# Kernel optimization log

Hardware: AMD Instinct MI355X
Metric: run time of the kernel (lower is better)

The kernel has to match this reference:

```python
import jax, jax.numpy as jnp
import numpy as np

N_NODES = 50000
N_EDGES = 800000
N_GRAPHS = 256
D = 256
L = 3
BN_EPS = 1e-5


def setup_inputs() -> dict:
    key = jax.random.key(0)
    ks = jax.random.split(key, 8)
    x = jax.random.normal(ks[0], (N_NODES, D), dtype=jnp.float32)
    edge_index = jax.random.randint(ks[1], (2, N_EDGES), 0, N_NODES, dtype=jnp.int64)
    batch = jnp.sort(jax.random.randint(ks[2], (N_NODES,), 0, N_GRAPHS, dtype=jnp.int64))
    # small init scale keeps ReLU/BN chain numerically tame
    w1 = jax.random.normal(ks[3], (L, D, D), dtype=jnp.float32) * 0.05
    b1 = jnp.zeros((L, D), dtype=jnp.float32)
    w2 = jax.random.normal(ks[4], (L, D, D), dtype=jnp.float32) * 0.05
    b2 = jnp.zeros((L, D), dtype=jnp.float32)
    gamma = jnp.ones((L, D), dtype=jnp.float32)
    beta = jnp.zeros((L, D), dtype=jnp.float32)
    return {"x": x, "edge_index": edge_index, "batch": batch,
            "w1": w1, "b1": b1, "w2": w2, "b2": b2,
            "gamma": gamma, "beta": beta}


def reference(x, edge_index, batch, w1, b1, w2, b2, gamma, beta):
    src = edge_index[0]  # message senders (x_j)
    dst = edge_index[1]  # aggregation targets (x_i)
    h = x
    xs = []
    for i in range(L):
        # GINConv (eps=0): MLP(x_i + sum_{j in N(i)} x_j)
        agg = jax.ops.segment_sum(h[src], dst, num_segments=N_NODES)  # [N, D]
        z = h + agg
        z = jnp.maximum(z @ w1[i] + b1[i], 0.0) @ w2[i] + b2[i]  # Linear-ReLU-Linear
        z = jnp.maximum(z, 0.0)  # F.relu after conv
        # BatchNorm1d (training mode: biased batch stats over nodes)
        mean = jnp.mean(z, axis=0)
        var = jnp.var(z, axis=0)
        z = (z - mean) * jax.lax.rsqrt(var + BN_EPS) * gamma[i] + beta[i]
        xs.append(z)
        h = z
    # global_add_pool per layer, then concat along features -> [G, L*D]
    pooled = [jax.ops.segment_sum(xi, batch, num_segments=N_GRAPHS) for xi in xs]
    return jnp.concatenate(pooled, axis=1)
```

## Files before the change

kernel.cpp:

```cpp
#include <hip/hip_runtime.h>

#define NN 50000
#define NE 800000
#define NG 256
#define DD 256
#define NL 3
#define BN_EPS 1e-5f
#define MPAD 50048
#define CAP 96
#define NMB 391

typedef short bf16x8 __attribute__((ext_vector_type(8)));
typedef float f32x4 __attribute__((ext_vector_type(4)));
typedef unsigned short ushort8 __attribute__((ext_vector_type(8)));

__device__ __forceinline__ unsigned short f2bf(float f) {
    unsigned int u = __float_as_uint(f);
    u += 0x7FFFu + ((u >> 16) & 1u);
    return (unsigned short)(u >> 16);
}
__device__ __forceinline__ float bf2f(unsigned short s) {
    return __uint_as_float(((unsigned int)s) << 16);
}

__global__ void k_init(int* __restrict__ deg) {
    int i = blockIdx.x * blockDim.x + threadIdx.x;
    if (i < NN) deg[i] = 0;
}

__global__ void k_scatter(const int* __restrict__ ei, int* __restrict__ deg,
                          unsigned short* __restrict__ elist) {
    int e = blockIdx.x * blockDim.x + threadIdx.x;
    if (e >= NE) return;
    int s = ei[e];
    int d = ei[NE + e];
    int pos = atomicAdd(&deg[d], 1);
    elist[(size_t)d * CAP + pos] = (unsigned short)s;
}

__global__ void k_gbounds(const int* __restrict__ batch, int* __restrict__ gstart) {
    int g = threadIdx.x;
    int lo = 0, hi = NN;
    while (lo < hi) {
        int mid = (lo + hi) >> 1;
        if (batch[mid] < g) lo = mid + 1; else hi = mid;
    }
    gstart[g] = lo;
    if (g == 0) gstart[NG] = NN;
}

__global__ void k_f2bf(const float* __restrict__ in, unsigned short* __restrict__ out, int n4) {
    int i = blockIdx.x * blockDim.x + threadIdx.x;
    if (i >= n4) return;
    float4 v = ((const float4*)in)[i];
    ushort4 o;
    o.x = f2bf(v.x); o.y = f2bf(v.y); o.z = f2bf(v.z); o.w = f2bf(v.w);
    ((ushort4*)out)[i] = o;
}

__global__ void k_zrow(unsigned short* __restrict__ hbf) {
    hbf[(size_t)NN * DD + threadIdx.x] = 0;
}

__global__ void k_zpad(unsigned short* p) {
    int i = blockIdx.x * blockDim.x + threadIdx.x;
    const int total = (MPAD - NN) * DD;
    if (i < total) p[NN * DD + i] = 0;
}

__global__ void k_wconv(const float* __restrict__ w1, const float* __restrict__ w2,
                        unsigned short* __restrict__ wt) {
    int flat = blockIdx.x * blockDim.x + threadIdx.x;
    if (flat >= 6 * 65536) return;
    int mat = flat >> 16;
    int n = (flat >> 8) & 255;
    int k = flat & 255;
    const float* src = (mat < 3) ? (w1 + ((size_t)mat << 16)) : (w2 + ((size_t)(mat - 3) << 16));
    wt[flat] = f2bf(src[k * 256 + n]);
}

__global__ __launch_bounds__(256) void k_agg_bf(const unsigned short* __restrict__ h,
                                                const int* __restrict__ deg,
                                                const unsigned short* __restrict__ elist,
                                                unsigned short* __restrict__ z0) {
    int wave = threadIdx.x >> 6;
    int lane = threadIdx.x & 63;
    int node = blockIdx.x * 4 + wave;
    int chunk = lane & 31;
    int half = lane >> 5;
    const ushort8* h8 = (const ushort8*)h;

    float acc[8];
    if (half == 0) {
        ushort8 own = h8[(size_t)node * 32 + chunk];
        #pragma unroll
        for (int j = 0; j < 8; ++j) acc[j] = bf2f(own[j]);
    } else {
        #pragma unroll
        for (int j = 0; j < 8; ++j) acc[j] = 0.f;
    }

    int n = deg[node];
    const unsigned short* el = elist + (size_t)node * CAP;
    int i = 0;
    for (; i + 8 <= n; i += 8) {
        ushort8 sv = *(const ushort8*)(el + i);
        int i0 = half ? sv[1] : sv[0];
        int i1 = half ? sv[3] : sv[2];
        int i2 = half ? sv[5] : sv[4];
        int i3 = half ? sv[7] : sv[6];
        ushort8 r0 = h8[(size_t)i0 * 32 + chunk];
        ushort8 r1 = h8[(size_t)i1 * 32 + chunk];
        ushort8 r2 = h8[(size_t)i2 * 32 + chunk];
        ushort8 r3 = h8[(size_t)i3 * 32 + chunk];
        #pragma unroll
        for (int j = 0; j < 8; ++j) acc[j] += bf2f(r0[j]);
        #pragma unroll
        for (int j = 0; j < 8; ++j) acc[j] += bf2f(r1[j]);
        #pragma unroll
        for (int j = 0; j < 8; ++j) acc[j] += bf2f(r2[j]);
        #pragma unroll
        for (int j = 0; j < 8; ++j) acc[j] += bf2f(r3[j]);
    }
    for (; i < n; i += 2) {
        int s0 = el[i];
        int s1 = (i + 1 < n) ? (int)el[i + 1] : NN;
        int idx = half ? s1 : s0;
        ushort8 r = h8[(size_t)idx * 32 + chunk];
        #pragma unroll
        for (int j = 0; j < 8; ++j) acc[j] += bf2f(r[j]);
    }

    ushort8 o;
    #pragma unroll
    for (int j = 0; j < 8; ++j) {
        float other = __shfl_xor(acc[j], 32);
        o[j] = f2bf(acc[j] + other);
    }
    if (half == 0) ((ushort8*)z0)[(size_t)node * 32 + chunk] = o;
}

__global__ __launch_bounds__(512, 2) void k_mlp(const unsigned short* __restrict__ A,
                                                const unsigned short* __restrict__ BT1,
                                                const unsigned short* __restrict__ BT2,
                                                const float* __restrict__ b1,
                                                const float* __restrict__ b2,
                                                float* __restrict__ Cout,
                                                float* __restrict__ pstat) {
    __shared__ short As[128 * 64];
    __shared__ short Bs[256 * 64];
    __shared__ short H1[128 * 256];
    __shared__ float spart[2][256][2];
    int tid = threadIdx.x;
    int lane = tid & 63;
    int wave = tid >> 6;
    int wr = wave >> 2, wc = wave & 3;
    long m0 = (long)blockIdx.x * 128;
    const int r = lane & 15, hi = lane >> 4;

    f32x4 acc[4][4];
    #pragma unroll
    for (int m = 0; m < 4; ++m)
        #pragma unroll
        for (int n = 0; n < 4; ++n)
            acc[m][n] = (f32x4){0.f, 0.f, 0.f, 0.f};

    for (int k0 = 0; k0 < DD; k0 += 64) {
        #pragma unroll
        for (int p = 0; p < 2; ++p) {
            int flat = p * 512 + tid;
            int row = flat >> 3, c8 = flat & 7;
            int slot = c8 ^ (row & 7);
            *(bf16x8*)(As + row * 64 + slot * 8) =
                *(const bf16x8*)(A + (m0 + row) * DD + k0 + c8 * 8);
        }
        #pragma unroll
        for (int p = 0; p < 4; ++p) {
            int flat = p * 512 + tid;
            int row = flat >> 3, c8 = flat & 7;
            int slot = c8 ^ (row & 7);
            *(bf16x8*)(Bs + row * 64 + slot * 8) =
                *(const bf16x8*)(BT1 + (long)row * DD + k0 + c8 * 8);
        }
        __syncthreads();
        bf16x8 af[4][2], bfr[4][2];
        #pragma unroll
        for (int m = 0; m < 4; ++m) {
            int row = wr * 64 + m * 16 + r;
            #pragma unroll
            for (int kk = 0; kk < 2; ++kk) {
                int slot = (kk * 4 + hi) ^ (row & 7);
                af[m][kk] = *(const bf16x8*)(As + row * 64 + slot * 8);
            }
        }
        #pragma unroll
        for (int n = 0; n < 4; ++n) {
            int col = wc * 64 + n * 16 + r;
            #pragma unroll
            for (int kk = 0; kk < 2; ++kk) {
                int slot = (kk * 4 + hi) ^ (col & 7);
                bfr[n][kk] = *(const bf16x8*)(Bs + col * 64 + slot * 8);
            }
        }
        #pragma unroll
        for (int kk = 0; kk < 2; ++kk)
            #pragma unroll
            for (int m = 0; m < 4; ++m)
                #pragma unroll
                for (int n = 0; n < 4; ++n)
                    acc[m][n] = __builtin_amdgcn_mfma_f32_16x16x32_bf16(af[m][kk], bfr[n][kk], acc[m][n], 0, 0, 0);
        __syncthreads();
    }

    #pragma unroll
    for (int n = 0; n < 4; ++n) {
        int col = wc * 64 + n * 16 + r;
        float bv = b1[col];
        int g = col >> 3, j8 = col & 7;
        #pragma unroll
        for (int m = 0; m < 4; ++m) {
            #pragma unroll
            for (int j = 0; j < 4; ++j) {
                int row = wr * 64 + m * 16 + hi * 4 + j;
                float v = acc[m][n][j] + bv;
                v = v > 0.f ? v : 0.f;
                H1[row * 256 + (g ^ (row & 7)) * 8 + j8] = (short)f2bf(v);
            }
        }
    }
    #pragma unroll
    for (int m = 0; m < 4; ++m)
        #pragma unroll
        for (int n = 0; n < 4; ++n)
            acc[m][n] = (f32x4){0.f, 0.f, 0.f, 0.f};
    __syncthreads();

    for (int k0 = 0; k0 < DD; k0 += 64) {
        #pragma unroll
        for (int p = 0; p < 4; ++p) {
            int flat = p * 512 + tid;
            int row = flat >> 3, c8 = flat & 7;
            int slot = c8 ^ (row & 7);
            *(bf16x8*)(Bs + row * 64 + slot * 8) =
                *(const bf16x8*)(BT2 + (long)row * DD + k0 + c8 * 8);
        }
        __syncthreads();
        bf16x8 af[4][2], bfr[4][2];
        #pragma unroll
        for (int m = 0; m < 4; ++m) {
            int row = wr * 64 + m * 16 + r;
            #pragma unroll
            for (int kk = 0; kk < 2; ++kk) {
                int g = (k0 >> 3) + kk * 4 + hi;
                af[m][kk] = *(const bf16x8*)(H1 + row * 256 + (g ^ (row & 7)) * 8);
            }
        }
        #pragma unroll
        for (int n = 0; n < 4; ++n) {
            int col = wc * 64 + n * 16 + r;
            #pragma unroll
            for (int kk = 0; kk < 2; ++kk) {
                int slot = (kk * 4 + hi) ^ (col & 7);
                bfr[n][kk] = *(const bf16x8*)(Bs + col * 64 + slot * 8);
            }
        }
        #pragma unroll
        for (int kk = 0; kk < 2; ++kk)
            #pragma unroll
            for (int m = 0; m < 4; ++m)
                #pragma unroll
                for (int n = 0; n < 4; ++n)
                    acc[m][n] = __builtin_amdgcn_mfma_f32_16x16x32_bf16(af[m][kk], bfr[n][kk], acc[m][n], 0, 0, 0);
        __syncthreads();
    }

    #pragma unroll
    for (int n = 0; n < 4; ++n) {
        int col = wc * 64 + n * 16 + r;
        float bv = b2[col];
        float cs = 0.f, cs2 = 0.f;
        #pragma unroll
        for (int m = 0; m < 4; ++m) {
            #pragma unroll
            for (int j = 0; j < 4; ++j) {
                long grow = m0 + wr * 64 + m * 16 + hi * 4 + j;
                float v = acc[m][n][j] + bv;
                v = v > 0.f ? v : 0.f;
                Cout[grow * DD + col] = v;
                float vm = (grow < NN) ? v : 0.f;
                cs += vm; cs2 += vm * vm;
            }
        }
        cs  += __shfl_xor(cs, 16);  cs  += __shfl_xor(cs, 32);
        cs2 += __shfl_xor(cs2, 16); cs2 += __shfl_xor(cs2, 32);
        if (hi == 0) {
            spart[wr][col][0] = cs;
            spart[wr][col][1] = cs2;
        }
    }
    __syncthreads();
    if (tid < 256) {
        float s  = spart[0][tid][0] + spart[1][tid][0];
        float s2 = spart[0][tid][1] + spart[1][tid][1];
        pstat[(size_t)blockIdx.x * 512 + tid] = s;
        pstat[(size_t)blockIdx.x * 512 + 256 + tid] = s2;
    }
}

__global__ __launch_bounds__(256) void k_bnscale2(const float* __restrict__ pstat,
                                                  const float* __restrict__ gamma,
                                                  const float* __restrict__ beta,
                                                  float* __restrict__ ss) {
    int c = blockIdx.x;
    int t = threadIdx.x;
    float s = 0.f, s2 = 0.f;
    for (int mb = t; mb < NMB; mb += 256) {
        s  += pstat[(size_t)mb * 512 + c];
        s2 += pstat[(size_t)mb * 512 + 256 + c];
    }
    __shared__ float rs[256], rs2[256];
    rs[t] = s; rs2[t] = s2;
    __syncthreads();
    #pragma unroll
    for (int d = 128; d > 0; d >>= 1) {
        if (t < d) { rs[t] += rs[t + d]; rs2[t] += rs2[t + d]; }
        __syncthreads();
    }
    if (t == 0) {
        float mean = rs[0] * (1.0f / NN);
        float var = rs2[0] * (1.0f / NN) - mean * mean;
        float sc = gamma[c] * rsqrtf(var + BN_EPS);
        ss[c] = sc;
        ss[DD + c] = beta[c] - mean * sc;
    }
}

__global__ __launch_bounds__(512) void k_bnpool(const float* __restrict__ z,
                                                const float* __restrict__ ss,
                                                const int* __restrict__ gstart,
                                                unsigned short* __restrict__ hbf,
                                                float* __restrict__ out, int layer) {
    __shared__ float4 red[8][64];
    int g = blockIdx.x;
    int t = threadIdx.x;
    int q = t & 63, rg = t >> 6;
    float4 sc = ((const float4*)ss)[q];
    float4 sh = ((const float4*)(ss + DD))[q];
    int lo = gstart[g], hi = gstart[g + 1];
    float4 s = {0.f, 0.f, 0.f, 0.f};
    const float4* z4 = (const float4*)z;
    ushort4* h4 = (ushort4*)hbf;
    for (int r = lo + rg; r < hi; r += 8) {
        float4 v = z4[r * 64 + q];
        v.x = v.x * sc.x + sh.x;
        v.y = v.y * sc.y + sh.y;
        v.z = v.z * sc.z + sh.z;
        v.w = v.w * sc.w + sh.w;
        s.x += v.x; s.y += v.y; s.z += v.z; s.w += v.w;
        ushort4 o;
        o.x = f2bf(v.x); o.y = f2bf(v.y); o.z = f2bf(v.z); o.w = f2bf(v.w);
        h4[r * 64 + q] = o;
    }
    red[rg][q] = s;
    __syncthreads();
    if (rg < 4) {
        float4 a = red[rg][q], b = red[rg + 4][q];
        a.x += b.x; a.y += b.y; a.z += b.z; a.w += b.w;
        red[rg][q] = a;
    }
    __syncthreads();
    if (rg < 2) {
        float4 a = red[rg][q], b = red[rg + 2][q];
        a.x += b.x; a.y += b.y; a.z += b.z; a.w += b.w;
        red[rg][q] = a;
    }
    __syncthreads();
    if (rg == 0) {
        float4 a = red[0][q], b = red[1][q];
        a.x += b.x; a.y += b.y; a.z += b.z; a.w += b.w;
        ((float4*)(out + (size_t)g * (NL * DD) + layer * DD))[q] = a;
    }
}

extern "C" void kernel_launch(void* const* d_in, const int* in_sizes, int n_in,
                              void* d_out, int out_size, void* d_ws, size_t ws_size,
                              hipStream_t stream) {
    const float* x     = (const float*)d_in[0];
    const int*   ei    = (const int*)d_in[1];
    const int*   batch = (const int*)d_in[2];
    const float* w1    = (const float*)d_in[3];
    const float* b1    = (const float*)d_in[4];
    const float* w2    = (const float*)d_in[5];
    const float* b2    = (const float*)d_in[6];
    const float* gamma = (const float*)d_in[7];
    const float* beta  = (const float*)d_in[8];
    float* out = (float*)d_out;

    char* ws = (char*)d_ws;
    size_t off = 0;
    auto alloc = [&](size_t bytes) -> void* {
        void* p = ws + off;
        off += (bytes + 255) & ~size_t(255);
        return p;
    };
    float*          buf0 = (float*)alloc((size_t)MPAD * DD * 4);
    unsigned short* zbf  = (unsigned short*)alloc((size_t)MPAD * DD * 2);
    unsigned short* hbf  = (unsigned short*)alloc((size_t)(NN + 64) * DD * 2);
    unsigned short* wt   = (unsigned short*)alloc((size_t)6 * DD * DD * 2);
    int* deg    = (int*)alloc((size_t)NN * 4);
    unsigned short* elist = (unsigned short*)alloc((size_t)NN * CAP * 2);
    int* gstart = (int*)alloc((size_t)(NG + 1) * 4);
    float* pstat = (float*)alloc((size_t)NMB * 512 * 4);
    float* ss   = (float*)alloc(2 * DD * 4);

    k_init<<<(NN + 255) / 256, 256, 0, stream>>>(deg);
    k_scatter<<<(NE + 255) / 256, 256, 0, stream>>>(ei, deg, elist);
    k_gbounds<<<1, 256, 0, stream>>>(batch, gstart);

    k_wconv<<<(6 * 65536 + 255) / 256, 256, 0, stream>>>(w1, w2, wt);
    k_f2bf<<<(NN * DD / 4 + 255) / 256, 256, 0, stream>>>(x, hbf, NN * DD / 4);
    k_zrow<<<1, 256, 0, stream>>>(hbf);
    k_zpad<<<((MPAD - NN) * DD + 255) / 256, 256, 0, stream>>>(zbf);

    for (int l = 0; l < NL; ++l) {
        k_agg_bf<<<NN / 4, 256, 0, stream>>>(hbf, deg, elist, zbf);
        k_mlp<<<NMB, 512, 0, stream>>>(zbf, wt + (size_t)l * DD * DD,
                                       wt + (size_t)(3 + l) * DD * DD,
                                       b1 + l * DD, b2 + l * DD, buf0, pstat);
        k_bnscale2<<<DD, 256, 0, stream>>>(pstat, gamma + l * DD, beta + l * DD, ss);
        k_bnpool<<<NG, 512, 0, stream>>>(buf0, ss, gstart, hbf, out, l);
    }
}
```

Baseline: 419.9 us.

## Fuse setup kernels, split aggregation by feature halves, widen bnpool grid

Merges the separate setup kernels (bf16 conversion, weight transpose, zeroing, graph bounds) into one launch to cut launch overhead. Aggregation now runs as two launches, each covering half of the feature columns with four edges gathered in parallel per wave, so each pass touches a smaller working set of h that may fit better in cache. The BN+pool kernel uses a 2D grid over graph and feature half, and the final layer skips writing the bf16 hidden state that no later kernel reads. The cost is a second pass over the edge lists, extra shuffle reductions, and one more launch per layer.

```diff
diff --git a/kernel.cpp b/kernel.cpp
--- a/kernel.cpp
+++ b/kernel.cpp
@@ -23,9 +23,53 @@
     return __uint_as_float(((unsigned int)s) << 16);
 }
 
-__global__ void k_init(int* __restrict__ deg) {
+#define R0 3200000
+#define R1 393216
+#define R2 50000
+#define R3 12288
+#define R4 256
+#define R5 256
+#define RTOT (R0 + R1 + R2 + R3 + R4 + R5)
+
+__global__ void k_setup(const float* __restrict__ x, const float* __restrict__ w1,
+                        const float* __restrict__ w2, const int* __restrict__ batch,
+                        unsigned short* __restrict__ hbf, unsigned short* __restrict__ wt,
+                        int* __restrict__ deg, unsigned short* __restrict__ zbf,
+                        int* __restrict__ gstart) {
     int i = blockIdx.x * blockDim.x + threadIdx.x;
-    if (i < NN) deg[i] = 0;
+    if (i < R0) {
+        float4 v = ((const float4*)x)[i];
+        ushort4 o;
+        o.x = f2bf(v.x); o.y = f2bf(v.y); o.z = f2bf(v.z); o.w = f2bf(v.w);
+        ((ushort4*)hbf)[i] = o;
+        return;
+    }
+    i -= R0;
+    if (i < R1) {
+        int mat = i >> 16;
+        int n = (i >> 8) & 255;
+        int k = i & 255;
+        const float* src = (mat < 3) ? (w1 + ((size_t)mat << 16)) : (w2 + ((size_t)(mat - 3) << 16));
+        wt[i] = f2bf(src[k * 256 + n]);
+        return;
+    }
+    i -= R1;
+    if (i < R2) { deg[i] = 0; return; }
+    i -= R2;
+    if (i < R3) { zbf[NN * DD + i] = 0; return; }
+    i -= R3;
+    if (i < R4) { hbf[(size_t)NN * DD + i] = 0; return; }
+    i -= R4;
+    if (i < R5) {
+        int g = i;
+        int lo = 0, hi = NN;
+        while (lo < hi) {
+            int mid = (lo + hi) >> 1;
+            if (batch[mid] < g) lo = mid + 1; else hi = mid;
+        }
+        gstart[g] = lo;
+        if (g == 0) gstart[NG] = NN;
+    }
 }
 
 __global__ void k_scatter(const int* __restrict__ ei, int* __restrict__ deg,
@@ -38,47 +82,7 @@
     elist[(size_t)d * CAP + pos] = (unsigned short)s;
 }
 
-__global__ void k_gbounds(const int* __restrict__ batch, int* __restrict__ gstart) {
-    int g = threadIdx.x;
-    int lo = 0, hi = NN;
-    while (lo < hi) {
-        int mid = (lo + hi) >> 1;
-        if (batch[mid] < g) lo = mid + 1; else hi = mid;
-    }
-    gstart[g] = lo;
-    if (g == 0) gstart[NG] = NN;
-}
-
-__global__ void k_f2bf(const float* __restrict__ in, unsigned short* __restrict__ out, int n4) {
-    int i = blockIdx.x * blockDim.x + threadIdx.x;
-    if (i >= n4) return;
-    float4 v = ((const float4*)in)[i];
-    ushort4 o;
-    o.x = f2bf(v.x); o.y = f2bf(v.y); o.z = f2bf(v.z); o.w = f2bf(v.w);
-    ((ushort4*)out)[i] = o;
-}
-
-__global__ void k_zrow(unsigned short* __restrict__ hbf) {
-    hbf[(size_t)NN * DD + threadIdx.x] = 0;
-}
-
-__global__ void k_zpad(unsigned short* p) {
-    int i = blockIdx.x * blockDim.x + threadIdx.x;
-    const int total = (MPAD - NN) * DD;
-    if (i < total) p[NN * DD + i] = 0;
-}
-
-__global__ void k_wconv(const float* __restrict__ w1, const float* __restrict__ w2,
-                        unsigned short* __restrict__ wt) {
-    int flat = blockIdx.x * blockDim.x + threadIdx.x;
-    if (flat >= 6 * 65536) return;
-    int mat = flat >> 16;
-    int n = (flat >> 8) & 255;
-    int k = flat & 255;
-    const float* src = (mat < 3) ? (w1 + ((size_t)mat << 16)) : (w2 + ((size_t)(mat - 3) << 16));
-    wt[flat] = f2bf(src[k * 256 + n]);
-}
-
+template<int HALF>
 __global__ __launch_bounds__(256) void k_agg_bf(const unsigned short* __restrict__ h,
                                                 const int* __restrict__ deg,
                                                 const unsigned short* __restrict__ elist,
@@ -86,13 +90,14 @@
     int wave = threadIdx.x >> 6;
     int lane = threadIdx.x & 63;
     int node = blockIdx.x * 4 + wave;
-    int chunk = lane & 31;
-    int half = lane >> 5;
+    int chunk = lane & 15;
+    int eway = lane >> 4;
+    const int base = HALF * 16 + chunk;
     const ushort8* h8 = (const ushort8*)h;
 
     float acc[8];
-    if (half == 0) {
-        ushort8 own = h8[(size_t)node * 32 + chunk];
+    if (eway == 0) {
+        ushort8 own = h8[(size_t)node * 32 + base];
         #pragma unroll
         for (int j = 0; j < 8; ++j) acc[j] = bf2f(own[j]);
     } else {
@@ -105,28 +110,19 @@
     int i = 0;
     for (; i + 8 <= n; i += 8) {
         ushort8 sv = *(const ushort8*)(el + i);
-        int i0 = half ? sv[1] : sv[0];
-        int i1 = half ? sv[3] : sv[2];
-        int i2 = half ? sv[5] : sv[4];
-        int i3 = half ? sv[7] : sv[6];
-        ushort8 r0 = h8[(size_t)i0 * 32 + chunk];
-        ushort8 r1 = h8[(size_t)i1 * 32 + chunk];
-        ushort8 r2 = h8[(size_t)i2 * 32 + chunk];
-        ushort8 r3 = h8[(size_t)i3 * 32 + chunk];
+        int i0 = sv[eway];
+        int i1 = sv[eway + 4];
+        ushort8 r0 = h8[(size_t)i0 * 32 + base];
+        ushort8 r1 = h8[(size_t)i1 * 32 + base];
         #pragma unroll
         for (int j = 0; j < 8; ++j) acc[j] += bf2f(r0[j]);
         #pragma unroll
         for (int j = 0; j < 8; ++j) acc[j] += bf2f(r1[j]);
-        #pragma unroll
-        for (int j = 0; j < 8; ++j) acc[j] += bf2f(r2[j]);
-        #pragma unroll
-        for (int j = 0; j < 8; ++j) acc[j] += bf2f(r3[j]);
-    }
-    for (; i < n; i += 2) {
-        int s0 = el[i];
-        int s1 = (i + 1 < n) ? (int)el[i + 1] : NN;
-        int idx = half ? s1 : s0;
-        ushort8 r = h8[(size_t)idx * 32 + chunk];
+    }
+    for (; i < n; i += 4) {
+        int e = i + eway;
+        int idx = (e < n) ? (int)el[e] : NN;
+        ushort8 r = h8[(size_t)idx * 32 + base];
         #pragma unroll
         for (int j = 0; j < 8; ++j) acc[j] += bf2f(r[j]);
     }
@@ -134,10 +130,12 @@
     ushort8 o;
     #pragma unroll
     for (int j = 0; j < 8; ++j) {
-        float other = __shfl_xor(acc[j], 32);
-        o[j] = f2bf(acc[j] + other);
-    }
-    if (half == 0) ((ushort8*)z0)[(size_t)node * 32 + chunk] = o;
+        float v = acc[j];
+        v += __shfl_xor(v, 16);
+        v += __shfl_xor(v, 32);
+        o[j] = f2bf(v);
+    }
+    if (eway == 0) ((ushort8*)z0)[(size_t)node * 32 + base] = o;
 }
 
 __global__ __launch_bounds__(512, 2) void k_mlp(const unsigned short* __restrict__ A,
@@ -335,50 +333,50 @@
     }
 }
 
+template<int LAST>
 __global__ __launch_bounds__(512) void k_bnpool(const float* __restrict__ z,
                                                 const float* __restrict__ ss,
                                                 const int* __restrict__ gstart,
                                                 unsigned short* __restrict__ hbf,
                                                 float* __restrict__ out, int layer) {
-    __shared__ float4 red[8][64];
+    __shared__ float4 red[16][32];
     int g = blockIdx.x;
+    int ch = blockIdx.y;
     int t = threadIdx.x;
-    int q = t & 63, rg = t >> 6;
-    float4 sc = ((const float4*)ss)[q];
-    float4 sh = ((const float4*)(ss + DD))[q];
+    int q = t & 31, rg = t >> 5;
+    int cq = ch * 32 + q;
+    float4 sc = ((const float4*)ss)[cq];
+    float4 sh = ((const float4*)(ss + DD))[cq];
     int lo = gstart[g], hi = gstart[g + 1];
     float4 s = {0.f, 0.f, 0.f, 0.f};
     const float4* z4 = (const float4*)z;
     ushort4* h4 = (ushort4*)hbf;
-    for (int r = lo + rg; r < hi; r += 8) {
-        float4 v = z4[r * 64 + q];
+    for (int r = lo + rg; r < hi; r += 16) {
+        float4 v = z4[(size_t)r * 64 + cq];
         v.x = v.x * sc.x + sh.x;
         v.y = v.y * sc.y + sh.y;
         v.z = v.z * sc.z + sh.z;
         v.w = v.w * sc.w + sh.w;
         s.x += v.x; s.y += v.y; s.z += v.z; s.w += v.w;
-        ushort4 o;
-        o.x = f2bf(v.x); o.y = f2bf(v.y); o.z = f2bf(v.z); o.w = f2bf(v.w);
-        h4[r * 64 + q] = o;
+        if (!LAST) {
+            ushort4 o;
+            o.x = f2bf(v.x); o.y = f2bf(v.y); o.z = f2bf(v.z); o.w = f2bf(v.w);
+            h4[(size_t)r * 64 + cq] = o;
+        }
     }
     red[rg][q] = s;
     __syncthreads();
-    if (rg < 4) {
-        float4 a = red[rg][q], b = red[rg + 4][q];
-        a.x += b.x; a.y += b.y; a.z += b.z; a.w += b.w;
-        red[rg][q] = a;
-    }
-    __syncthreads();
-    if (rg < 2) {
-        float4 a = red[rg][q], b = red[rg + 2][q];
-        a.x += b.x; a.y += b.y; a.z += b.z; a.w += b.w;
-        red[rg][q] = a;
-    }
-    __syncthreads();
+    #pragma unroll
+    for (int d = 8; d > 0; d >>= 1) {
+        if (rg < d) {
+            float4 a = red[rg][q], b = red[rg + d][q];
+            a.x += b.x; a.y += b.y; a.z += b.z; a.w += b.w;
+            red[rg][q] = a;
+        }
+        __syncthreads();
+    }
     if (rg == 0) {
-        float4 a = red[0][q], b = red[1][q];
-        a.x += b.x; a.y += b.y; a.z += b.z; a.w += b.w;
-        ((float4*)(out + (size_t)g * (NL * DD) + layer * DD))[q] = a;
+        ((float4*)(out + (size_t)g * (NL * DD) + layer * DD))[cq] = red[0][q];
     }
 }
 
@@ -413,21 +411,19 @@
     float* pstat = (float*)alloc((size_t)NMB * 512 * 4);
     float* ss   = (float*)alloc(2 * DD * 4);
 
-    k_init<<<(NN + 255) / 256, 256, 0, stream>>>(deg);
+    k_setup<<<(RTOT + 255) / 256, 256, 0, stream>>>(x, w1, w2, batch, hbf, wt, deg, zbf, gstart);
     k_scatter<<<(NE + 255) / 256, 256, 0, stream>>>(ei, deg, elist);
-    k_gbounds<<<1, 256, 0, stream>>>(batch, gstart);
-
-    k_wconv<<<(6 * 65536 + 255) / 256, 256, 0, stream>>>(w1, w2, wt);
-    k_f2bf<<<(NN * DD / 4 + 255) / 256, 256, 0, stream>>>(x, hbf, NN * DD / 4);
-    k_zrow<<<1, 256, 0, stream>>>(hbf);
-    k_zpad<<<((MPAD - NN) * DD + 255) / 256, 256, 0, stream>>>(zbf);
 
     for (int l = 0; l < NL; ++l) {
-        k_agg_bf<<<NN / 4, 256, 0, stream>>>(hbf, deg, elist, zbf);
+        k_agg_bf<0><<<NN / 4, 256, 0, stream>>>(hbf, deg, elist, zbf);
+        k_agg_bf<1><<<NN / 4, 256, 0, stream>>>(hbf, deg, elist, zbf);
         k_mlp<<<NMB, 512, 0, stream>>>(zbf, wt + (size_t)l * DD * DD,
                                        wt + (size_t)(3 + l) * DD * DD,
                                        b1 + l * DD, b2 + l * DD, buf0, pstat);
         k_bnscale2<<<DD, 256, 0, stream>>>(pstat, gamma + l * DD, beta + l * DD, ss);
-        k_bnpool<<<NG, 512, 0, stream>>>(buf0, ss, gstart, hbf, out, l);
-    }
-}
+        if (l < NL - 1)
+            k_bnpool<0><<<dim3(NG, 2), 512, 0, stream>>>(buf0, ss, gstart, hbf, out, l);
+        else
+            k_bnpool<1><<<dim3(NG, 2), 512, 0, stream>>>(buf0, ss, gstart, hbf, out, l);
+    }
+}
```

Result: no change. 416.5 us (-0.8%).
